# Kernel tuning notes

Hardware: AMD Instinct MI355X
Metric: run time of the kernel (lower is better)

The kernel has to match this reference:

```python
import jax, jax.numpy as jnp
import numpy as np

TEMPERATURE = 1.0
W_BLEND = 0.8
EPS = 1e-12  # torch F.normalize eps


def _l2norm(x):
    n = jnp.sqrt(jnp.sum(x * x, axis=-1, keepdims=True))
    return x / jnp.maximum(n, EPS)


def setup_inputs() -> dict:
    key = jax.random.key(0)
    feats = jax.random.normal(key, (4, 2048, 256), dtype=jnp.float32)
    return {"feats": feats}


def reference(feats):
    B, N, C = feats.shape
    f = _l2norm(feats.reshape(B * N, C))                 # [BN, C], unit rows
    scores = jnp.matmul(f, f.T) / TEMPERATURE            # [BN, BN] cosine sims
    attn = jax.nn.softmax(scores, axis=-1)               # [BN, BN]
    feats_att = jnp.matmul(attn, f)                      # [BN, C]
    feats_fcm = f * W_BLEND + feats_att * (1.0 - W_BLEND)
    return _l2norm(feats_fcm.reshape(B, N, C))           # [B, N, C]
```

## Files before the change

### kernel.cpp

```cpp
#include <hip/hip_runtime.h>

typedef unsigned char u8;
typedef unsigned short u16;
typedef unsigned int u32;
typedef unsigned long long u64;
typedef long long i64;
typedef __attribute__((ext_vector_type(16))) float floatx16;
typedef __attribute__((ext_vector_type(4))) int intx4;
typedef __attribute__((ext_vector_type(8))) int intx8;

#define BN 8192
#define DIM 256
#define NSPLIT 8
#define KPS (BN / NSPLIT)
#define BKN 32
#define NIT (KPS / BKN)

__device__ __forceinline__ u16 f2bf(float x) {
    u32 u = __builtin_bit_cast(u32, x);
    u = (u + 0x7fffu + ((u >> 16) & 1u)) >> 16;
    return (u16)u;
}
__device__ __forceinline__ float bf2f(u16 h) {
    return __builtin_bit_cast(float, (u32)h << 16);
}
__device__ __forceinline__ u64 pack4bf(float a, float b, float c, float d) {
    return (u64)f2bf(a) | ((u64)f2bf(b) << 16) | ((u64)f2bf(c) << 32) | ((u64)f2bf(d) << 48);
}
__device__ __forceinline__ u32 pk_fp8(float a, float b, float c, float d) {
    int v = __builtin_amdgcn_cvt_pk_fp8_f32(a, b, 0, false);
    v = __builtin_amdgcn_cvt_pk_fp8_f32(c, d, v, true);
    return (u32)v;
}
__device__ __forceinline__ void gl_lds16(const void* g, void* l) {
    __builtin_amdgcn_global_load_lds(
        (const __attribute__((address_space(1))) u32*)g,
        (__attribute__((address_space(3))) u32*)l, 16, 0, 0);
}
#define MFMA8(A, B, C) __builtin_amdgcn_mfma_f32_32x32x16_fp8_fp8((A), (B), (C), 0, 0, 0)
#define MFMA64S(A, B, C) __builtin_amdgcn_mfma_scale_f32_32x32x64_f8f6f4( \
        (A), (B), (C), 0, 0, 0, (int)0x7f7f7f7f, 0, (int)0x7f7f7f7f)

__global__ __launch_bounds__(256) void k_prep(const float* __restrict__ in,
                                              u8* __restrict__ fb, u8* __restrict__ fv) {
    __shared__ u16 t[32 * 260];
    const int tid = threadIdx.x;
    const int wave = tid >> 6, lane = tid & 63;
    const int kb = blockIdx.x, r0 = kb * 32;
    #pragma unroll
    for (int i = 0; i < 8; ++i) {
        const int rl = wave * 8 + i;
        const float4 v = *(const float4*)(in + (size_t)(r0 + rl) * DIM + lane * 4);
        float ss = v.x * v.x + v.y * v.y + v.z * v.z + v.w * v.w;
        #pragma unroll
        for (int off = 1; off < 64; off <<= 1) ss += __shfl_xor(ss, off, 64);
        const float inv = 1.0f / fmaxf(sqrtf(ss), 1e-12f);
        const float n0 = v.x * inv, n1 = v.y * inv, n2 = v.z * inv, n3 = v.w * inv;
        *(u32*)(fb + (size_t)(r0 + rl) * DIM + lane * 4) = pk_fp8(n0, n1, n2, n3);
        *(u64*)(&t[rl * 260 + lane * 4]) = pack4bf(n0, n1, n2, n3);
    }
    __syncthreads();
    #pragma unroll
    for (int i = 0; i < 4; ++i) {
        const int S = i * 256 + tid;
        const int d = S >> 2;
        const int c = ((S & 3) - (d >> 2)) & 3;
        float f[8];
        #pragma unroll
        for (int j = 0; j < 8; ++j) f[j] = bf2f(t[(8 * c + j) * 260 + d]);
        const u32 lo = pk_fp8(f[0], f[1], f[2], f[3]);
        const u32 hi = pk_fp8(f[4], f[5], f[6], f[7]);
        *(u64*)(fv + (size_t)kb * 8192 + S * 8) = ((u64)hi << 32) | lo;
    }
}

__global__ __launch_bounds__(256, 2) void k_flash(
        const u8* __restrict__ fb, const u8* __restrict__ fv,
        u16* __restrict__ Opart, float* __restrict__ lpart) {
    __shared__ u8 tileK[2][8192];
    __shared__ u8 tileV[2][8192];

    const int tid = threadIdx.x;
    const int wave = tid >> 6, lane = tid & 63;
    const int c31 = lane & 31, g1 = lane >> 5;
    const int split = blockIdx.x & (NSPLIT - 1);
    const int qblk = blockIdx.x >> 3;
    const int q0 = qblk * 128 + wave * 32;
    const int key0 = split * KPS;

    intx8 qf[4];
    #pragma unroll
    for (int g = 0; g < 4; ++g) {
        const u8* qb = fb + (size_t)(q0 + c31) * DIM + g * 64 + g1 * 32;
        const intx4 lo = *(const intx4*)(qb);
        const intx4 hi = *(const intx4*)(qb + 16);
        qf[g] = __builtin_shufflevector(lo, hi, 0, 1, 2, 3, 4, 5, 6, 7);
    }

    floatx16 o[8];
    #pragma unroll
    for (int i = 0; i < 8; ++i)
        #pragma unroll
        for (int r = 0; r < 16; ++r) o[i][r] = 0.f;
    float lsum = 0.f;

    int offK[2];
    #pragma unroll
    for (int i = 0; i < 2; ++i) {
        const int S = wave * 128 + i * 64 + lane;
        const int r = S >> 4, s = S & 15;
        const int c = (s & 8) | ((s ^ r) & 7);
        offK[i] = r * 256 + c * 16;
    }
    const u8* gK = fb + (size_t)key0 * DIM;
    const u8* gV = fv + (size_t)(key0 >> 5) * 8192;

    auto stage = [&](int s, int b) {
        const size_t oo = (size_t)s * 8192;
        u8* lK = &tileK[b][0] + wave * 2048;
        u8* lV = &tileV[b][0] + wave * 2048;
        #pragma unroll
        for (int i = 0; i < 2; ++i) gl_lds16(gK + oo + offK[i], lK + i * 1024);
        #pragma unroll
        for (int i = 0; i < 2; ++i)
            gl_lds16(gV + oo + wave * 2048 + i * 1024 + lane * 16, lV + i * 1024);
    };

    const int cswA = (g1 + (c31 >> 2)) & 3;
    const int cswB = (2 + g1 + (c31 >> 2)) & 3;

    stage(0, 0);
    for (int it = 0; it < NIT; ++it) {
        const int b = it & 1;
        __syncthreads();
        if (it + 1 < NIT) stage(it + 1, b ^ 1);

        const u8* tk = &tileK[b][0];
        const u8* tv = &tileV[b][0];
        const u8* bk = tk + c31 * 256;

        auto ldk = [&](int g) -> intx8 {
            const int cw = g * 4 + g1 * 2;
            const int sl = (cw & 8) | ((cw ^ c31) & 7);
            const intx4 lo = *(const intx4*)(bk + sl * 16);
            const intx4 hi = *(const intx4*)(bk + (sl ^ 1) * 16);
            return __builtin_shufflevector(lo, hi, 0, 1, 2, 3, 4, 5, 6, 7);
        };

        floatx16 s;
        #pragma unroll
        for (int r = 0; r < 16; ++r) s[r] = 0.f;

        i64 vfa[8], vfb[8];
        intx8 ka0 = ldk(0);
        intx8 ka1 = ldk(1);
        #pragma unroll
        for (int dp = 0; dp < 4; ++dp) {
            const u8* ba = tv + (((dp * 2) * 32 + c31) * 4 + cswA) * 8;
            vfa[2 * dp] = *(const i64*)(ba);
            vfa[2 * dp + 1] = *(const i64*)(ba + 1024);
        }
        s = MFMA64S(ka0, qf[0], s);
        ka0 = ldk(2);
        s = MFMA64S(ka1, qf[1], s);
        ka1 = ldk(3);
        #pragma unroll
        for (int dp = 0; dp < 4; ++dp) {
            const u8* ba = tv + (((dp * 2) * 32 + c31) * 4 + cswB) * 8;
            vfb[2 * dp] = *(const i64*)(ba);
            vfb[2 * dp + 1] = *(const i64*)(ba + 1024);
        }
        s = MFMA64S(ka0, qf[2], s);
        s = MFMA64S(ka1, qf[3], s);

        const float e0 = __expf(s[0]), e1 = __expf(s[1]), e2 = __expf(s[2]), e3 = __expf(s[3]);
        const float e4 = __expf(s[4]), e5 = __expf(s[5]), e6 = __expf(s[6]), e7 = __expf(s[7]);
        const u32 p0 = pk_fp8(e0, e1, e2, e3);
        const u32 p1 = pk_fp8(e4, e5, e6, e7);
        const u32 x0 = (u32)__shfl_xor((int)(g1 ? p0 : p1), 32, 64);
        const i64 A0 = g1 ? (i64)(((u64)p1 << 32) | x0) : (i64)(((u64)x0 << 32) | p0);

        o[0] = MFMA8(A0, vfa[0], o[0]);
        const float e8 = __expf(s[8]), e9 = __expf(s[9]);
        o[1] = MFMA8(A0, vfa[1], o[1]);
        const float e10 = __expf(s[10]), e11 = __expf(s[11]);
        o[2] = MFMA8(A0, vfa[2], o[2]);
        const float e12 = __expf(s[12]), e13 = __expf(s[13]);
        o[3] = MFMA8(A0, vfa[3], o[3]);
        const float e14 = __expf(s[14]), e15 = __expf(s[15]);
        o[4] = MFMA8(A0, vfa[4], o[4]);
        const u32 p2 = pk_fp8(e8, e9, e10, e11);
        lsum += (e0 + e1) + (e2 + e3);
        o[5] = MFMA8(A0, vfa[5], o[5]);
        const u32 p3 = pk_fp8(e12, e13, e14, e15);
        lsum += (e4 + e5) + (e6 + e7);
        o[6] = MFMA8(A0, vfa[6], o[6]);
        const u32 x1 = (u32)__shfl_xor((int)(g1 ? p2 : p3), 32, 64);
        lsum += (e8 + e9) + (e10 + e11);
        o[7] = MFMA8(A0, vfa[7], o[7]);
        const i64 A1 = g1 ? (i64)(((u64)p3 << 32) | x1) : (i64)(((u64)x1 << 32) | p2);
        lsum += (e12 + e13) + (e14 + e15);

        #pragma unroll
        for (int ds = 0; ds < 8; ++ds) o[ds] = MFMA8(A1, vfb[ds], o[ds]);
    }

    u16* ob = Opart + ((size_t)split * BN + q0) * DIM;
    #pragma unroll
    for (int ds = 0; ds < 8; ++ds) {
        #pragma unroll
        for (int r = 0; r < 16; ++r) {
            const int ql = (r & 3) + 8 * (r >> 2) + 4 * g1;
            ob[(size_t)ql * DIM + ds * 32 + c31] = f2bf(o[ds][r]);
        }
    }
    lsum += __shfl_xor(lsum, 32, 64);
    if (g1 == 0) lpart[(size_t)split * BN + q0 + c31] = lsum;
}

__global__ __launch_bounds__(256) void k_combine(
        const float* __restrict__ feats, const u16* __restrict__ Opart,
        const float* __restrict__ lpart, float* __restrict__ out) {
    const int row = blockIdx.x * 4 + (threadIdx.x >> 6);
    const int lane = threadIdx.x & 63;

    float L = 0.f;
    #pragma unroll
    for (int s = 0; s < NSPLIT; ++s) L += lpart[(size_t)s * BN + row];

    float a0 = 0.f, a1 = 0.f, a2 = 0.f, a3 = 0.f;
    #pragma unroll
    for (int s = 0; s < NSPLIT; ++s) {
        const ushort4 o = *(const ushort4*)(Opart + ((size_t)s * BN + row) * DIM + lane * 4);
        a0 += bf2f(o.x); a1 += bf2f(o.y); a2 += bf2f(o.z); a3 += bf2f(o.w);
    }
    const float invL = 1.0f / L;

    const float4 v = *(const float4*)(feats + (size_t)row * DIM + lane * 4);
    float ss = v.x * v.x + v.y * v.y + v.z * v.z + v.w * v.w;
    #pragma unroll
    for (int off = 1; off < 64; off <<= 1) ss += __shfl_xor(ss, off, 64);
    const float invf = 1.0f / fmaxf(sqrtf(ss), 1e-12f);

    const float yx = 0.8f * v.x * invf + 0.2f * a0 * invL;
    const float yy = 0.8f * v.y * invf + 0.2f * a1 * invL;
    const float yz = 0.8f * v.z * invf + 0.2f * a2 * invL;
    const float yw = 0.8f * v.w * invf + 0.2f * a3 * invL;

    float s2 = yx * yx + yy * yy + yz * yz + yw * yw;
    #pragma unroll
    for (int off = 1; off < 64; off <<= 1) s2 += __shfl_xor(s2, off, 64);
    const float invn = 1.0f / fmaxf(sqrtf(s2), 1e-12f);

    float4 o; o.x = yx * invn; o.y = yy * invn; o.z = yz * invn; o.w = yw * invn;
    *(float4*)(out + (size_t)row * DIM + lane * 4) = o;
}

extern "C" void kernel_launch(void* const* d_in, const int* in_sizes, int n_in,
                              void* d_out, int out_size, void* d_ws, size_t ws_size,
                              hipStream_t stream) {
    const float* feats = (const float*)d_in[0];
    float* out = (float*)d_out;
    char* ws = (char*)d_ws;

    u8* fb = (u8*)ws;
    u8* fv = (u8*)(ws + (size_t)BN * DIM);
    u16* Op = (u16*)(ws + (size_t)BN * DIM * 2);
    float* lp = (float*)(ws + (size_t)BN * DIM * 2 + (size_t)NSPLIT * BN * DIM * 2);

    k_prep<<<BN / 32, 256, 0, stream>>>(feats, fb, fv);
    k_flash<<<(BN / 128) * NSPLIT, 256, 0, stream>>>(fb, fv, Op, lp);
    k_combine<<<BN / 4, 256, 0, stream>>>(feats, Op, lp, out);
}
```

Measured before the change: 119.9 us.

## Double key tile to 64 and use K=64 scaled MFMA for PV product

Doubles the key block per iteration from 32 to 64, so each iteration computes two 32x32 score tiles and feeds the fp8 probabilities into the 32x32x64 scaled MFMA for the P·V product. This replaces sixteen 32x32x16 fp8 MFMAs with eight K=64 ones. It also halves the number of loop iterations and barriers. In exchange LDS use per block doubles to 64 KB and register pressure rises, which may lower occupancy below the two blocks per CU requested by the launch bounds.

```diff
diff --git a/kernel.cpp b/kernel.cpp
--- a/kernel.cpp
+++ b/kernel.cpp
@@ -13,7 +13,7 @@
 #define DIM 256
 #define NSPLIT 8
 #define KPS (BN / NSPLIT)
-#define BKN 32
+#define BKN 64
 #define NIT (KPS / BKN)
 
 __device__ __forceinline__ u16 f2bf(float x) {
@@ -37,7 +37,6 @@
         (const __attribute__((address_space(1))) u32*)g,
         (__attribute__((address_space(3))) u32*)l, 16, 0, 0);
 }
-#define MFMA8(A, B, C) __builtin_amdgcn_mfma_f32_32x32x16_fp8_fp8((A), (B), (C), 0, 0, 0)
 #define MFMA64S(A, B, C) __builtin_amdgcn_mfma_scale_f32_32x32x64_f8f6f4( \
         (A), (B), (C), 0, 0, 0, (int)0x7f7f7f7f, 0, (int)0x7f7f7f7f)
 
@@ -77,8 +76,8 @@
 __global__ __launch_bounds__(256, 2) void k_flash(
         const u8* __restrict__ fb, const u8* __restrict__ fv,
         u16* __restrict__ Opart, float* __restrict__ lpart) {
-    __shared__ u8 tileK[2][8192];
-    __shared__ u8 tileV[2][8192];
+    __shared__ u8 tileK[2][16384];
+    __shared__ u8 tileV[2][16384];
 
     const int tid = threadIdx.x;
     const int wave = tid >> 6, lane = tid & 63;
@@ -104,10 +103,10 @@
         for (int r = 0; r < 16; ++r) o[i][r] = 0.f;
     float lsum = 0.f;
 
-    int offK[2];
-    #pragma unroll
-    for (int i = 0; i < 2; ++i) {
-        const int S = wave * 128 + i * 64 + lane;
+    int offK[4];
+    #pragma unroll
+    for (int i = 0; i < 4; ++i) {
+        const int S = wave * 256 + i * 64 + lane;
         const int r = S >> 4, s = S & 15;
         const int c = (s & 8) | ((s ^ r) & 7);
         offK[i] = r * 256 + c * 16;
@@ -116,18 +115,20 @@
     const u8* gV = fv + (size_t)(key0 >> 5) * 8192;
 
     auto stage = [&](int s, int b) {
-        const size_t oo = (size_t)s * 8192;
-        u8* lK = &tileK[b][0] + wave * 2048;
-        u8* lV = &tileV[b][0] + wave * 2048;
-        #pragma unroll
-        for (int i = 0; i < 2; ++i) gl_lds16(gK + oo + offK[i], lK + i * 1024);
-        #pragma unroll
-        for (int i = 0; i < 2; ++i)
-            gl_lds16(gV + oo + wave * 2048 + i * 1024 + lane * 16, lV + i * 1024);
+        const size_t oo = (size_t)s * 16384;
+        u8* lK = &tileK[b][0];
+        u8* lV = &tileV[b][0] + wave * 4096;
+        #pragma unroll
+        for (int i = 0; i < 4; ++i)
+            gl_lds16(gK + oo + offK[i], lK + wave * 4096 + i * 1024);
+        #pragma unroll
+        for (int i = 0; i < 4; ++i)
+            gl_lds16(gV + oo + wave * 4096 + i * 1024 + lane * 16, lV + i * 1024);
     };
 
-    const int cswA = (g1 + (c31 >> 2)) & 3;
-    const int cswB = (2 + g1 + (c31 >> 2)) & 3;
+    const int rot = c31 >> 2;
+    const int co0 = ((rot) & 3) * 8, co1 = ((1 + rot) & 3) * 8;
+    const int co2 = ((2 + rot) & 3) * 8, co3 = ((3 + rot) & 3) * 8;
 
     stage(0, 0);
     for (int it = 0; it < NIT; ++it) {
@@ -136,73 +137,93 @@
         if (it + 1 < NIT) stage(it + 1, b ^ 1);
 
         const u8* tk = &tileK[b][0];
-        const u8* tv = &tileV[b][0];
-        const u8* bk = tk + c31 * 256;
-
-        auto ldk = [&](int g) -> intx8 {
+        const u8* bk0 = tk + c31 * 256;
+        const u8* bk1 = tk + 8192 + c31 * 256;
+        const u8* vbase = &tileV[b][0] + g1 * 8192 + c31 * 32;
+
+        auto ldk = [&](const u8* bk, int g) -> intx8 {
             const int cw = g * 4 + g1 * 2;
             const int sl = (cw & 8) | ((cw ^ c31) & 7);
             const intx4 lo = *(const intx4*)(bk + sl * 16);
             const intx4 hi = *(const intx4*)(bk + (sl ^ 1) * 16);
             return __builtin_shufflevector(lo, hi, 0, 1, 2, 3, 4, 5, 6, 7);
         };
-
-        floatx16 s;
-        #pragma unroll
-        for (int r = 0; r < 16; ++r) s[r] = 0.f;
-
-        i64 vfa[8], vfb[8];
-        intx8 ka0 = ldk(0);
-        intx8 ka1 = ldk(1);
-        #pragma unroll
-        for (int dp = 0; dp < 4; ++dp) {
-            const u8* ba = tv + (((dp * 2) * 32 + c31) * 4 + cswA) * 8;
-            vfa[2 * dp] = *(const i64*)(ba);
-            vfa[2 * dp + 1] = *(const i64*)(ba + 1024);
-        }
-        s = MFMA64S(ka0, qf[0], s);
-        ka0 = ldk(2);
-        s = MFMA64S(ka1, qf[1], s);
-        ka1 = ldk(3);
-        #pragma unroll
-        for (int dp = 0; dp < 4; ++dp) {
-            const u8* ba = tv + (((dp * 2) * 32 + c31) * 4 + cswB) * 8;
-            vfb[2 * dp] = *(const i64*)(ba);
-            vfb[2 * dp + 1] = *(const i64*)(ba + 1024);
-        }
-        s = MFMA64S(ka0, qf[2], s);
-        s = MFMA64S(ka1, qf[3], s);
-
-        const float e0 = __expf(s[0]), e1 = __expf(s[1]), e2 = __expf(s[2]), e3 = __expf(s[3]);
-        const float e4 = __expf(s[4]), e5 = __expf(s[5]), e6 = __expf(s[6]), e7 = __expf(s[7]);
-        const u32 p0 = pk_fp8(e0, e1, e2, e3);
-        const u32 p1 = pk_fp8(e4, e5, e6, e7);
-        const u32 x0 = (u32)__shfl_xor((int)(g1 ? p0 : p1), 32, 64);
-        const i64 A0 = g1 ? (i64)(((u64)p1 << 32) | x0) : (i64)(((u64)x0 << 32) | p0);
-
-        o[0] = MFMA8(A0, vfa[0], o[0]);
-        const float e8 = __expf(s[8]), e9 = __expf(s[9]);
-        o[1] = MFMA8(A0, vfa[1], o[1]);
-        const float e10 = __expf(s[10]), e11 = __expf(s[11]);
-        o[2] = MFMA8(A0, vfa[2], o[2]);
-        const float e12 = __expf(s[12]), e13 = __expf(s[13]);
-        o[3] = MFMA8(A0, vfa[3], o[3]);
-        const float e14 = __expf(s[14]), e15 = __expf(s[15]);
-        o[4] = MFMA8(A0, vfa[4], o[4]);
-        const u32 p2 = pk_fp8(e8, e9, e10, e11);
-        lsum += (e0 + e1) + (e2 + e3);
-        o[5] = MFMA8(A0, vfa[5], o[5]);
-        const u32 p3 = pk_fp8(e12, e13, e14, e15);
-        lsum += (e4 + e5) + (e6 + e7);
-        o[6] = MFMA8(A0, vfa[6], o[6]);
-        const u32 x1 = (u32)__shfl_xor((int)(g1 ? p2 : p3), 32, 64);
-        lsum += (e8 + e9) + (e10 + e11);
-        o[7] = MFMA8(A0, vfa[7], o[7]);
-        const i64 A1 = g1 ? (i64)(((u64)p3 << 32) | x1) : (i64)(((u64)x1 << 32) | p2);
-        lsum += (e12 + e13) + (e14 + e15);
-
-        #pragma unroll
-        for (int ds = 0; ds < 8; ++ds) o[ds] = MFMA8(A1, vfb[ds], o[ds]);
+        auto ldv = [&](int ds) -> intx8 {
+            const u8* vb = vbase + ds * 1024;
+            const i64 v0 = *(const i64*)(vb + co0);
+            const i64 v1 = *(const i64*)(vb + co1);
+            const i64 v2 = *(const i64*)(vb + co2);
+            const i64 v3 = *(const i64*)(vb + co3);
+            intx8 r;
+            r[0] = (int)v0; r[1] = (int)(v0 >> 32);
+            r[2] = (int)v1; r[3] = (int)(v1 >> 32);
+            r[4] = (int)v2; r[5] = (int)(v2 >> 32);
+            r[6] = (int)v3; r[7] = (int)(v3 >> 32);
+            return r;
+        };
+
+        floatx16 s0, s1;
+        #pragma unroll
+        for (int r = 0; r < 16; ++r) { s0[r] = 0.f; s1[r] = 0.f; }
+
+        intx8 ka0 = ldk(bk0, 0);
+        intx8 ka1 = ldk(bk0, 1);
+        s0 = MFMA64S(ka0, qf[0], s0); ka0 = ldk(bk0, 2);
+        s0 = MFMA64S(ka1, qf[1], s0); ka1 = ldk(bk0, 3);
+        s0 = MFMA64S(ka0, qf[2], s0); ka0 = ldk(bk1, 0);
+        s0 = MFMA64S(ka1, qf[3], s0); ka1 = ldk(bk1, 1);
+
+        s1 = MFMA64S(ka0, qf[0], s1);
+        const float f00 = __expf(s0[0]), f01 = __expf(s0[1]), f02 = __expf(s0[2]), f03 = __expf(s0[3]);
+        const float f04 = __expf(s0[4]), f05 = __expf(s0[5]), f06 = __expf(s0[6]), f07 = __expf(s0[7]);
+        ka0 = ldk(bk1, 2);
+        s1 = MFMA64S(ka1, qf[1], s1);
+        const float f08 = __expf(s0[8]), f09 = __expf(s0[9]), f10 = __expf(s0[10]), f11 = __expf(s0[11]);
+        const float f12 = __expf(s0[12]), f13 = __expf(s0[13]), f14 = __expf(s0[14]), f15 = __expf(s0[15]);
+        ka1 = ldk(bk1, 3);
+        s1 = MFMA64S(ka0, qf[2], s1);
+        const u32 pA0 = pk_fp8(f00, f01, f02, f03);
+        const u32 pA1 = pk_fp8(f04, f05, f06, f07);
+        const u32 pA2 = pk_fp8(f08, f09, f10, f11);
+        const u32 pA3 = pk_fp8(f12, f13, f14, f15);
+        lsum += ((f00 + f01) + (f02 + f03)) + ((f04 + f05) + (f06 + f07));
+        lsum += ((f08 + f09) + (f10 + f11)) + ((f12 + f13) + (f14 + f15));
+        s1 = MFMA64S(ka1, qf[3], s1);
+
+        const float g00 = __expf(s1[0]), g01 = __expf(s1[1]), g02 = __expf(s1[2]), g03 = __expf(s1[3]);
+        const float g04 = __expf(s1[4]), g05 = __expf(s1[5]), g06 = __expf(s1[6]), g07 = __expf(s1[7]);
+        const float g08 = __expf(s1[8]), g09 = __expf(s1[9]), g10 = __expf(s1[10]), g11 = __expf(s1[11]);
+        const float g12 = __expf(s1[12]), g13 = __expf(s1[13]), g14 = __expf(s1[14]), g15 = __expf(s1[15]);
+        const u32 pB0 = pk_fp8(g00, g01, g02, g03);
+        const u32 pB1 = pk_fp8(g04, g05, g06, g07);
+        const u32 pB2 = pk_fp8(g08, g09, g10, g11);
+        const u32 pB3 = pk_fp8(g12, g13, g14, g15);
+        lsum += ((g00 + g01) + (g02 + g03)) + ((g04 + g05) + (g06 + g07));
+        lsum += ((g08 + g09) + (g10 + g11)) + ((g12 + g13) + (g14 + g15));
+
+        const u32 tB0 = (u32)__shfl_xor((int)pB0, 32, 64);
+        const u32 uA0 = (u32)__shfl_xor((int)pA0, 32, 64);
+        const u32 tB1 = (u32)__shfl_xor((int)pB1, 32, 64);
+        const u32 uA1 = (u32)__shfl_xor((int)pA1, 32, 64);
+        const u32 tB2 = (u32)__shfl_xor((int)pB2, 32, 64);
+        const u32 uA2 = (u32)__shfl_xor((int)pA2, 32, 64);
+        const u32 tB3 = (u32)__shfl_xor((int)pB3, 32, 64);
+        const u32 uA3 = (u32)__shfl_xor((int)pA3, 32, 64);
+        intx8 PA;
+        PA[0] = (int)(g1 ? tB0 : pA0); PA[1] = (int)(g1 ? pB0 : uA0);
+        PA[2] = (int)(g1 ? tB1 : pA1); PA[3] = (int)(g1 ? pB1 : uA1);
+        PA[4] = (int)(g1 ? tB2 : pA2); PA[5] = (int)(g1 ? pB2 : uA2);
+        PA[6] = (int)(g1 ? tB3 : pA3); PA[7] = (int)(g1 ? pB3 : uA3);
+
+        intx8 v0 = ldv(0), v1 = ldv(1);
+        o[0] = MFMA64S(PA, v0, o[0]); v0 = ldv(2);
+        o[1] = MFMA64S(PA, v1, o[1]); v1 = ldv(3);
+        o[2] = MFMA64S(PA, v0, o[2]); v0 = ldv(4);
+        o[3] = MFMA64S(PA, v1, o[3]); v1 = ldv(5);
+        o[4] = MFMA64S(PA, v0, o[4]); v0 = ldv(6);
+        o[5] = MFMA64S(PA, v1, o[5]); v1 = ldv(7);
+        o[6] = MFMA64S(PA, v0, o[6]);
+        o[7] = MFMA64S(PA, v1, o[7]);
     }
 
     u16* ob = Opart + ((size_t)split * BN + q0) * DIM;
```

After: 114.4 us. 1.05x faster.
